# Kernel tuning notes

Measured on AMD Instinct MI355X. Metric: run time of the kernel, lower is better.

The kernel has to match this reference:

```python
import math
import jax, jax.numpy as jnp
import numpy as np

N, MA, DESIGN, RADIAL, SOFTENING, RM = 8, 24, 26, 15, 3, 5.0


def setup_inputs() -> dict:
    key = jax.random.key(0)
    k1, k2 = jax.random.split(key, 2)
    # atomic coordinates, spread out so interatomic distances are realistic (bohr)
    coords = jax.random.normal(k1, (N, MA, 3), jnp.float32) * 3.0
    # labels all >= 0 -> full padding (padding[i] == MA for every molecule)
    labels = jax.random.randint(k2, (N, MA), 0, 10)
    # deterministic synthetic Lebedev-like design (26 points on the unit sphere)
    phi = jnp.linspace(0.0, 2.0 * math.pi, DESIGN, endpoint=False).astype(jnp.float32)
    psi = jnp.linspace(0.1, math.pi - 0.1, DESIGN).astype(jnp.float32)
    sphere = jnp.stack([jnp.cos(phi) * jnp.sin(psi),
                        jnp.sin(phi) * jnp.sin(psi),
                        jnp.cos(psi)], axis=1)           # [D, 3]
    sphere_weights = jnp.full((DESIGN,), 1.0 / DESIGN, dtype=jnp.float32)
    return {"labels": labels, "coords": coords,
            "sphere": sphere, "sphere_weights": sphere_weights}


def _spheric_grid(sphere, sphere_weights):
    # Gauss-Chebyshev radial quadrature mapped by the Becke transform
    i = jnp.arange(1, RADIAL + 1, dtype=jnp.float32)
    z = -jnp.cos(math.pi * (2.0 * i - 1.0) / (2.0 * RADIAL))
    dr = 2.0 * RM * (1.0 - z) ** -2
    r = RM * (1.0 + z) / (1.0 - z)
    w = jnp.sqrt(1.0 - z ** 2) * dr * math.pi / RADIAL
    w = r ** 2 * 4.0 * math.pi * w                       # [R]
    conc = (r[:, None, None] * sphere[None]).reshape(-1, 3)          # [R*D, 3]
    wt = (sphere_weights[None, :] * w[:, None]).reshape(-1)          # [R*D]
    return conc, wt


def _becke(x, r, dm, idx):
    # x [n, mx, 3] grid points, r [n, M, 3] centers, dm [n, M, M], idx [mx]
    rx = jnp.linalg.norm(x[:, :, None, :] - r[:, None, :, :], axis=-1)   # [n, mx, M]
    # elliptic coordinate mu_ij for every grid point: [n, mx, M, M]
    mu = (rx[..., :, None] - rx[..., None, :]) / jnp.clip(dm[:, None], 1e-12, None)
    for _ in range(1, SOFTENING):                       # softening passes
        mu = 0.5 * mu * (3.0 - mu ** 2)
    mu = 0.5 * (1.0 - mu)
    mu = mu + 0.5 * jnp.eye(dm.shape[-1], dtype=x.dtype)  # diagonal -> 1
    cell = jnp.prod(mu, axis=-1)                        # [n, mx, M] cell functions
    v_i = jnp.take_along_axis(cell, idx[None, :, None], axis=2)[..., 0]
    return v_i / cell.sum(axis=2)


def reference(labels, coords, sphere, sphere_weights):
    # labels are all >= 0 here, so padding == MA for every molecule and the
    # original per-molecule loop collapses into one batched computation.
    conc, wt = _spheric_grid(sphere, sphere_weights)    # conc [ms,3], wt [ms]
    ms = conc.shape[0]
    n, M, _ = coords.shape
    dm = jnp.linalg.norm(coords[:, :, None, :] - coords[:, None, :, :], axis=-1)
    # place concentric spheres on each atom (atom-major ordering, as in torch)
    grid = (coords[:, :, None, :] + conc[None, None]).reshape(n, M * ms, 3)
    w_full = jnp.broadcast_to(wt[None, :], (M, ms)).reshape(-1)      # [M*ms]
    idx = jnp.repeat(jnp.arange(M), ms)                              # sample -> center
    v = _becke(grid, coords, dm, idx)                                # [n, M*ms]
    weights = v * w_full[None, :]
    dv = grid[:, :, None, :] - coords[:, None, :, :]                 # [n, M*ms, M, 3]
    return grid, dv, weights
```

## Files before the change

### kernel.cpp

```cpp
#include <hip/hip_runtime.h>
#include <math.h>

constexpr int MAC = 24;
constexpr int DES = 26;
constexpr int RAD = 15;
constexpr int MS  = RAD * DES;
constexpr int MX  = MAC * MS;
constexpr int PPG = 2;
constexpr int GPB = 8;
constexpr int PPB = PPG * GPB;
constexpr int BPM = MX / PPB;

typedef float v2f __attribute__((ext_vector_type(2)));

__device__ __forceinline__ v2f pk_fma(v2f a, v2f b, v2f c) {
    return __builtin_elementwise_fma(a, b, c);
}

template <int M>
__device__ __forceinline__ float xorswz(float v) {
    return __int_as_float(__builtin_amdgcn_ds_swizzle(__float_as_int(v), (M << 10) | 0x1f));
}
template <int CTRL>
__device__ __forceinline__ float dppx(float v) {
    return __int_as_float(__builtin_amdgcn_update_dpp(
        0, __float_as_int(v), CTRL, 0xf, 0xf, true));
}

__global__ __launch_bounds__(256) void becke_pre(
    const float* __restrict__ coords, const float* __restrict__ sphere,
    const float* __restrict__ sw, int nmol,
    float* __restrict__ inv_dm, float4* __restrict__ conc4, float4* __restrict__ cpad)
{
    const int e = blockIdx.x * 256 + threadIdx.x;
    const int nidm = nmol * MAC * MAC;
    if (e < nidm) {
        int n = e / (MAC * MAC), r0 = e - n * MAC * MAC;
        int i = r0 / MAC, j = r0 - i * MAC;
        const float* cb = coords + n * MAC * 3;
        float dx = cb[i * 3 + 0] - cb[j * 3 + 0];
        float dy = cb[i * 3 + 1] - cb[j * 3 + 1];
        float dz = cb[i * 3 + 2] - cb[j * 3 + 2];
        float dd = sqrtf(dx * dx + dy * dy + dz * dz);
        inv_dm[e] = 1.0f / fmaxf(dd, 1e-12f);
        return;
    }
    const int e2 = e - nidm;
    if (e2 < MS) {
        int k = e2 / DES, d = e2 - k * DES;
        double i   = (double)k + 1.0;
        double z   = -cos(M_PI * (2.0 * i - 1.0) / (2.0 * (double)RAD));
        double omz = 1.0 - z;
        double dr  = 10.0 / (omz * omz);
        double r   = 5.0 * (1.0 + z) / omz;
        double w1  = sqrt(1.0 - z * z) * dr * M_PI / (double)RAD;
        double w   = r * r * 4.0 * M_PI * w1;
        conc4[e2] = make_float4((float)(r * (double)sphere[d * 3 + 0]),
                                (float)(r * (double)sphere[d * 3 + 1]),
                                (float)(r * (double)sphere[d * 3 + 2]),
                                (float)((double)sw[d] * w));
        return;
    }
    const int e3 = e2 - MS;
    if (e3 < nmol * MAC) {
        cpad[e3] = make_float4(coords[e3 * 3 + 0], coords[e3 * 3 + 1],
                               coords[e3 * 3 + 2], 0.0f);
    }
}

__global__ __launch_bounds__(256, 4) void becke_main(
    const float4* __restrict__ cpad,
    const float*  __restrict__ inv_dm,
    const float4* __restrict__ conc4,
    float* __restrict__ og,
    float* __restrict__ odv,
    float* __restrict__ ow)
{
    __shared__ v2f rxp[GPB][32];

    const int tid = threadIdx.x;
    const int l   = tid & 31;
    const int grp = tid >> 5;
    const int b   = blockIdx.x;
    const int n   = b / BPM;
    const int bm  = b - n * BPM;
    const int s0  = bm * PPB + grp * PPG;
    const bool act = (l < MAC);
    const int  i   = act ? l : (MAC - 1);

    const float4 ci = cpad[n * MAC + i];

    int ap[PPG];
    float gx[PPG], gy[PPG], gz[PPG], wt[PPG], rx[PPG];
    const size_t sgb = (size_t)n * MX + s0;
    float* dvp = odv + (sgb * MAC + i) * 3;

    #pragma unroll
    for (int p = 0; p < PPG; ++p) {
        int sp = s0 + p;
        ap[p] = sp / MS;
        int tp = sp - ap[p] * MS;
        float4 cc = conc4[tp];
        float4 ca = cpad[n * MAC + ap[p]];
        gx[p] = ca.x + cc.x;
        gy[p] = ca.y + cc.y;
        gz[p] = ca.z + cc.z;
        wt[p] = cc.w;
        float dx = gx[p] - ci.x;
        float dy = gy[p] - ci.y;
        float dz = gz[p] - ci.z;
        if (act) {
            dvp[p * MAC * 3 + 0] = dx;
            dvp[p * MAC * 3 + 1] = dy;
            dvp[p * MAC * 3 + 2] = dz;
        }
        rx[p] = __builtin_amdgcn_sqrtf(dx * dx + dy * dy + dz * dz);
    }
    rxp[grp][l] = (v2f){rx[0], rx[1]};
    __builtin_amdgcn_wave_barrier();

    float inv[MAC];
    {
        const float* irow = inv_dm + (n * MAC + i) * MAC;
        #pragma unroll
        for (int q = 0; q < MAC / 4; ++q) {
            float4 v = *reinterpret_cast<const float4*>(irow + q * 4);
            inv[q * 4 + 0] = v.x; inv[q * 4 + 1] = v.y;
            inv[q * 4 + 2] = v.z; inv[q * 4 + 3] = v.w;
        }
    }

    const v2f cm05 = {-0.5f, -0.5f}, c15 = {1.5f, 1.5f}, c05 = {0.5f, 0.5f};
    const v2f rxi = {rx[0], rx[1]};
    v2f prod = {1.0f, 1.0f};

    #pragma unroll
    for (int jj = 0; jj < MAC / 2; ++jj) {
        float4 v4 = *reinterpret_cast<const float4*>(&rxp[grp][2 * jj]);
        const v2f iva = {inv[2 * jj],     inv[2 * jj]};
        const v2f ivb = {inv[2 * jj + 1], inv[2 * jj + 1]};
        v2f mu = (rxi - (v2f){v4.x, v4.y}) * iva;
        mu = mu * pk_fma(mu * mu, cm05, c15);
        mu = mu * pk_fma(mu * mu, cm05, c15);
        prod = prod * pk_fma(mu, cm05, c05);
        v2f mv = (rxi - (v2f){v4.z, v4.w}) * ivb;
        mv = mv * pk_fma(mv * mv, cm05, c15);
        mv = mv * pk_fma(mv * mv, cm05, c15);
        prod = prod * pk_fma(mv, cm05, c05);
    }

    const v2f cell = prod * (act ? (v2f){2.0f, 2.0f} : (v2f){0.0f, 0.0f});

    #pragma unroll
    for (int p = 0; p < PPG; ++p) {
        float c  = (p == 0) ? cell.x : cell.y;
        float su = c;
        su += dppx<0xB1>(su);
        su += dppx<0x4E>(su);
        su += dppx<0x141>(su);
        su += dppx<0x140>(su);
        su += xorswz<16>(su);
        if (l == ap[p])
            ow[sgb + p] = c * __builtin_amdgcn_rcpf(su) * wt[p];
    }

    if (l >= MAC && l < MAC + PPG) {
        int p = l - MAC;
        float* gp = og + (sgb + p) * 3;
        gp[0] = gx[p]; gp[1] = gy[p]; gp[2] = gz[p];
    }
}

extern "C" void kernel_launch(void* const* d_in, const int* in_sizes, int n_in,
                              void* d_out, int out_size, void* d_ws, size_t ws_size,
                              hipStream_t stream) {
    const float* coords = (const float*)d_in[1];
    const float* sphere = (const float*)d_in[2];
    const float* sw     = (const float*)d_in[3];

    const int nmol = in_sizes[1] / (MAC * 3);

    float*  ws     = (float*)d_ws;
    float*  inv_dm = ws;
    float4* conc4  = (float4*)(inv_dm + (size_t)nmol * MAC * MAC);
    float4* cpad   = conc4 + MS;

    float* o     = (float*)d_out;
    float* ogrid = o;
    float* odv   = ogrid + (size_t)nmol * MX * 3;
    float* owt   = odv + (size_t)nmol * MX * MAC * 3;

    const int pre_elems  = nmol * MAC * MAC + MS + nmol * MAC;
    const int pre_blocks = (pre_elems + 255) / 256;
    becke_pre<<<dim3(pre_blocks), dim3(256), 0, stream>>>(
        coords, sphere, sw, nmol, inv_dm, conc4, cpad);

    becke_main<<<dim3(nmol * BPM), dim3(256), 0, stream>>>(
        cpad, inv_dm, conc4, ogrid, odv, owt);
}
```

Measured before the change: 79.55 us.

## Fuse precompute kernel into main Becke kernel, recompute distances and radial grid inline

Removes the separate preprocessing launch. Each block now computes the 24x24 inverse interatomic distance table into shared memory and evaluates the radial quadrature nodes and weights inline, using hardware sin/cos/rcp in float (a tangent form) instead of double precision. This drops one kernel launch and the global round trip through workspace. In exchange every block redundantly computes 576 distances plus a __syncthreads, and float precision for the quadrature may change the results slightly.

After: 81.50 us. 2.4% more time.

```diff
diff --git a/kernel.cpp b/kernel.cpp
--- a/kernel.cpp
+++ b/kernel.cpp
@@ -6,9 +6,8 @@
 constexpr int RAD = 15;
 constexpr int MS  = RAD * DES;
 constexpr int MX  = MAC * MS;
-constexpr int PPG = 2;
 constexpr int GPB = 8;
-constexpr int PPB = PPG * GPB;
+constexpr int PPB = 2 * GPB;
 constexpr int BPM = MX / PPB;
 
 typedef float v2f __attribute__((ext_vector_type(2)));
@@ -27,88 +26,79 @@
         0, __float_as_int(v), CTRL, 0xf, 0xf, true));
 }
 
-__global__ __launch_bounds__(256) void becke_pre(
-    const float* __restrict__ coords, const float* __restrict__ sphere,
-    const float* __restrict__ sw, int nmol,
-    float* __restrict__ inv_dm, float4* __restrict__ conc4, float4* __restrict__ cpad)
-{
-    const int e = blockIdx.x * 256 + threadIdx.x;
-    const int nidm = nmol * MAC * MAC;
-    if (e < nidm) {
-        int n = e / (MAC * MAC), r0 = e - n * MAC * MAC;
-        int i = r0 / MAC, j = r0 - i * MAC;
-        const float* cb = coords + n * MAC * 3;
-        float dx = cb[i * 3 + 0] - cb[j * 3 + 0];
-        float dy = cb[i * 3 + 1] - cb[j * 3 + 1];
-        float dz = cb[i * 3 + 2] - cb[j * 3 + 2];
-        float dd = sqrtf(dx * dx + dy * dy + dz * dz);
-        inv_dm[e] = 1.0f / fmaxf(dd, 1e-12f);
-        return;
-    }
-    const int e2 = e - nidm;
-    if (e2 < MS) {
-        int k = e2 / DES, d = e2 - k * DES;
-        double i   = (double)k + 1.0;
-        double z   = -cos(M_PI * (2.0 * i - 1.0) / (2.0 * (double)RAD));
-        double omz = 1.0 - z;
-        double dr  = 10.0 / (omz * omz);
-        double r   = 5.0 * (1.0 + z) / omz;
-        double w1  = sqrt(1.0 - z * z) * dr * M_PI / (double)RAD;
-        double w   = r * r * 4.0 * M_PI * w1;
-        conc4[e2] = make_float4((float)(r * (double)sphere[d * 3 + 0]),
-                                (float)(r * (double)sphere[d * 3 + 1]),
-                                (float)(r * (double)sphere[d * 3 + 2]),
-                                (float)((double)sw[d] * w));
-        return;
-    }
-    const int e3 = e2 - MS;
-    if (e3 < nmol * MAC) {
-        cpad[e3] = make_float4(coords[e3 * 3 + 0], coords[e3 * 3 + 1],
-                               coords[e3 * 3 + 2], 0.0f);
-    }
-}
-
-__global__ __launch_bounds__(256, 4) void becke_main(
-    const float4* __restrict__ cpad,
-    const float*  __restrict__ inv_dm,
-    const float4* __restrict__ conc4,
+__global__ __launch_bounds__(256) void becke_fused(
+    const float* __restrict__ coords,
+    const float* __restrict__ sphere,
+    const float* __restrict__ sw,
     float* __restrict__ og,
     float* __restrict__ odv,
     float* __restrict__ ow)
 {
-    __shared__ v2f rxp[GPB][32];
+    __shared__ float inv_sh[MAC][32];
+    __shared__ v2f   rxp[GPB][32];
 
     const int tid = threadIdx.x;
-    const int l   = tid & 31;
-    const int grp = tid >> 5;
     const int b   = blockIdx.x;
     const int n   = b / BPM;
     const int bm  = b - n * BPM;
-    const int s0  = bm * PPB + grp * PPG;
+    const float* cb = coords + n * MAC * 3;
+
+    for (int e = tid; e < MAC * MAC; e += 256) {
+        int ii = e / MAC, jj = e - ii * MAC;
+        float dx = cb[ii * 3 + 0] - cb[jj * 3 + 0];
+        float dy = cb[ii * 3 + 1] - cb[jj * 3 + 1];
+        float dz = cb[ii * 3 + 2] - cb[jj * 3 + 2];
+        float dd = fmaxf(dx * dx + dy * dy + dz * dz, 1e-24f);
+        inv_sh[jj][ii] = __builtin_amdgcn_rcpf(__builtin_amdgcn_sqrtf(dd));
+    }
+    __syncthreads();
+
+    const int l   = tid & 31;
+    const int grp = tid >> 5;
+    const int s0  = bm * PPB + grp * 2;
     const bool act = (l < MAC);
     const int  i   = act ? l : (MAC - 1);
 
-    const float4 ci = cpad[n * MAC + i];
+    const float cix = cb[i * 3 + 0];
+    const float ciy = cb[i * 3 + 1];
+    const float ciz = cb[i * 3 + 2];
 
-    int ap[PPG];
-    float gx[PPG], gy[PPG], gz[PPG], wt[PPG], rx[PPG];
+    float inv[MAC];
+    #pragma unroll
+    for (int j = 0; j < MAC; ++j) inv[j] = inv_sh[j][i];
+
+    int ap[2];
+    float gx[2], gy[2], gz[2], wt[2], rx[2];
     const size_t sgb = (size_t)n * MX + s0;
     float* dvp = odv + (sgb * MAC + i) * 3;
 
     #pragma unroll
-    for (int p = 0; p < PPG; ++p) {
+    for (int p = 0; p < 2; ++p) {
         int sp = s0 + p;
         ap[p] = sp / MS;
-        int tp = sp - ap[p] * MS;
-        float4 cc = conc4[tp];
-        float4 ca = cpad[n * MAC + ap[p]];
-        gx[p] = ca.x + cc.x;
-        gy[p] = ca.y + cc.y;
-        gz[p] = ca.z + cc.z;
-        wt[p] = cc.w;
-        float dx = gx[p] - ci.x;
-        float dy = gy[p] - ci.y;
-        float dz = gz[p] - ci.z;
+        int t  = sp - ap[p] * MS;
+        int k  = t / DES;
+        int d  = t - k * DES;
+
+        float h  = (float)(2 * k + 1) * (1.0f / 120.0f);
+        float sn = __builtin_amdgcn_sinf(h);
+        float cn = __builtin_amdgcn_cosf(h);
+        float rc = __builtin_amdgcn_rcpf(cn);
+        float t1 = sn * rc;
+        float u  = t1 * t1;
+        float r  = 5.0f * u;
+        float w  = 328.98681f * u * u * t1 * rc * rc;
+        wt[p] = sw[d] * w;
+
+        float sx = sphere[d * 3 + 0], sy = sphere[d * 3 + 1], sz = sphere[d * 3 + 2];
+        const float* cap = cb + ap[p] * 3;
+        gx[p] = cap[0] + r * sx;
+        gy[p] = cap[1] + r * sy;
+        gz[p] = cap[2] + r * sz;
+
+        float dx = gx[p] - cix;
+        float dy = gy[p] - ciy;
+        float dz = gz[p] - ciz;
         if (act) {
             dvp[p * MAC * 3 + 0] = dx;
             dvp[p * MAC * 3 + 1] = dy;
@@ -118,17 +108,6 @@
     }
     rxp[grp][l] = (v2f){rx[0], rx[1]};
     __builtin_amdgcn_wave_barrier();
-
-    float inv[MAC];
-    {
-        const float* irow = inv_dm + (n * MAC + i) * MAC;
-        #pragma unroll
-        for (int q = 0; q < MAC / 4; ++q) {
-            float4 v = *reinterpret_cast<const float4*>(irow + q * 4);
-            inv[q * 4 + 0] = v.x; inv[q * 4 + 1] = v.y;
-            inv[q * 4 + 2] = v.z; inv[q * 4 + 3] = v.w;
-        }
-    }
 
     const v2f cm05 = {-0.5f, -0.5f}, c15 = {1.5f, 1.5f}, c05 = {0.5f, 0.5f};
     const v2f rxi = {rx[0], rx[1]};
@@ -152,7 +131,7 @@
     const v2f cell = prod * (act ? (v2f){2.0f, 2.0f} : (v2f){0.0f, 0.0f});
 
     #pragma unroll
-    for (int p = 0; p < PPG; ++p) {
+    for (int p = 0; p < 2; ++p) {
         float c  = (p == 0) ? cell.x : cell.y;
         float su = c;
         su += dppx<0xB1>(su);
@@ -164,7 +143,7 @@
             ow[sgb + p] = c * __builtin_amdgcn_rcpf(su) * wt[p];
     }
 
-    if (l >= MAC && l < MAC + PPG) {
+    if (l >= MAC && l < MAC + 2) {
         int p = l - MAC;
         float* gp = og + (sgb + p) * 3;
         gp[0] = gx[p]; gp[1] = gy[p]; gp[2] = gz[p];
@@ -180,21 +159,11 @@
 
     const int nmol = in_sizes[1] / (MAC * 3);
 
-    float*  ws     = (float*)d_ws;
-    float*  inv_dm = ws;
-    float4* conc4  = (float4*)(inv_dm + (size_t)nmol * MAC * MAC);
-    float4* cpad   = conc4 + MS;
-
     float* o     = (float*)d_out;
     float* ogrid = o;
     float* odv   = ogrid + (size_t)nmol * MX * 3;
     float* owt   = odv + (size_t)nmol * MX * MAC * 3;
 
-    const int pre_elems  = nmol * MAC * MAC + MS + nmol * MAC;
-    const int pre_blocks = (pre_elems + 255) / 256;
-    becke_pre<<<dim3(pre_blocks), dim3(256), 0, stream>>>(
-        coords, sphere, sw, nmol, inv_dm, conc4, cpad);
-
-    becke_main<<<dim3(nmol * BPM), dim3(256), 0, stream>>>(
-        cpad, inv_dm, conc4, ogrid, odv, owt);
+    becke_fused<<<dim3(nmol * BPM), dim3(256), 0, stream>>>(
+        coords, sphere, sw, ogrid, odv, owt);
 }
```
